# Kernel optimization log

Measured on AMD Instinct MI355X. Metric: run time of the kernel, lower is better.

## Reference

```python
import jax, jax.numpy as jnp
import numpy as np

B, S, D, H = 4, 2048, 1024, 16
HD = D // H

def setup_inputs() -> dict:
    key = jax.random.key(0)
    ks = jax.random.split(key, 5)
    x = jax.random.normal(ks[0], (B, S, D), dtype=jnp.float32)
    # learned params (torch Linear: y = x @ W.T + b)
    s1 = 1.0 / np.sqrt(D)
    Wqkv = jax.random.uniform(ks[1], (3 * D, D), jnp.float32, -s1, s1)
    bqkv = jax.random.uniform(ks[2], (3 * D,), jnp.float32, -s1, s1)
    Wproj = jax.random.uniform(ks[3], (D, D), jnp.float32, -s1, s1)
    bproj = jax.random.uniform(ks[4], (D,), jnp.float32, -s1, s1)
    # causal mask, broadcast over batch and heads; 0 -> masked
    mask = jnp.tril(jnp.ones((S, S), jnp.int32))[None, None]
    return {"x": x, "Wqkv": Wqkv, "bqkv": bqkv, "Wproj": Wproj, "bproj": bproj, "mask": mask}

def reference(x, Wqkv, bqkv, Wproj, bproj, mask):
    b, s, d = x.shape
    qkv = x @ Wqkv.T + bqkv                      # [B,S,3D]
    qkv = qkv.reshape(b, s, 3, H, HD).transpose(2, 0, 3, 1, 4)  # [3,B,H,S,HD]
    q, k, v = qkv[0], qkv[1], qkv[2]
    scores = jnp.einsum('bhqd,bhkd->bhqk', q, k) / np.sqrt(HD).astype(np.float32)
    scores = jnp.where(mask == 0, -jnp.inf, scores)
    attn = jax.nn.softmax(scores, axis=-1)
    ctx = jnp.einsum('bhqk,bhkd->bhqd', attn, v)  # [B,H,S,HD]
    ctx = ctx.transpose(0, 2, 1, 3).reshape(b, s, d)
    return ctx @ Wproj.T + bproj
```

## Files before the change

kernel.cpp:

```cpp
#include <hip/hip_runtime.h>
#include <stdint.h>

typedef __bf16 bf16;
typedef __bf16 bf16x4 __attribute__((ext_vector_type(4)));
typedef __bf16 bf16x8 __attribute__((ext_vector_type(8)));
typedef float f32x4 __attribute__((ext_vector_type(4)));
typedef short short4v __attribute__((ext_vector_type(4)));

#define NB 4
#define NS 2048
#define ND 1024
#define NH 16
#define NHD 64
#define QSCALE 0.1803368801111204f
#define FMAX   8.0f
#define CPITCH 136

typedef const __attribute__((address_space(1))) unsigned GU;
typedef __attribute__((address_space(3))) unsigned LU;

__device__ __forceinline__ bf16x8 load8f(const float* p) {
    float4 a = *(const float4*)p;
    float4 b = *(const float4*)(p + 4);
    bf16x8 r;
    r[0] = (bf16)a.x; r[1] = (bf16)a.y; r[2] = (bf16)a.z; r[3] = (bf16)a.w;
    r[4] = (bf16)b.x; r[5] = (bf16)b.y; r[6] = (bf16)b.z; r[7] = (bf16)b.w;
    return r;
}
__device__ __forceinline__ void store8(bf16* p, bf16x8 v) { *(bf16x8*)p = v; }
__device__ __forceinline__ void store8(float* p, bf16x8 v) {
    float4 a; a.x = (float)v[0]; a.y = (float)v[1]; a.z = (float)v[2]; a.w = (float)v[3];
    float4 b; b.x = (float)v[4]; b.y = (float)v[5]; b.z = (float)v[6]; b.w = (float)v[7];
    *(float4*)p = a; *(float4*)(p + 4) = b;
}

__device__ __forceinline__ f32x4 mfma16(bf16x4 a, bf16x4 b, f32x4 c) {
#ifdef __HIP_DEVICE_COMPILE__
#if __has_builtin(__builtin_amdgcn_mfma_f32_16x16x16bf16_1k)
    return __builtin_amdgcn_mfma_f32_16x16x16bf16_1k(
        __builtin_bit_cast(short4v, a), __builtin_bit_cast(short4v, b), c, 0, 0, 0);
#else
    f32x4 d;
    asm("v_mfma_f32_16x16x16_bf16 %0, %1, %2, %3"
        : "=v"(d) : "v"(a), "v"(b), "v"(c));
    return d;
#endif
#else
    return c;
#endif
}

__device__ __forceinline__ int sw(int row, int col) {
    return row * 72 + (col ^ (((row >> 2) & 3) * 16));
}

__global__ __launch_bounds__(256)
void convert_kernel(const float* __restrict__ s0, bf16* __restrict__ d0, int n0,
                    const float* __restrict__ s1, bf16* __restrict__ d1, int n1,
                    const float* __restrict__ s2, bf16* __restrict__ d2, int n2)
{
    int idx = (blockIdx.x * 256 + threadIdx.x) * 8;
    const float* s; bf16* d;
    if (idx < n0)              { s = s0 + idx;  d = d0 + idx; }
    else if ((idx -= n0) < n1) { s = s1 + idx;  d = d1 + idx; }
    else if ((idx -= n1) < n2) { s = s2 + idx;  d = d2 + idx; }
    else return;
    *(bf16x8*)d = load8f(s);
}

template<typename TO, int MODE>
__device__ __forceinline__ void gemm_epilogue(
    f32x4 (&acc)[4][4], bf16* Ls, const float* __restrict__ bias,
    TO* __restrict__ O0, bf16* __restrict__ O1, bf16* __restrict__ O2,
    int N, int m0, int n0, int tid)
{
    const int lane = tid & 63;
    const int w = tid >> 6, wm = w >> 1, wn = w & 1;
    const int lr = lane & 15, quad = lane >> 4;
    const int cls = (MODE == 0) ? (n0 >> 10) : 1;

    if (MODE == 0 && cls == 2) {
#pragma unroll
        for (int im = 0; im < 4; ++im) {
            int rowb = wm * 64 + im * 16 + quad * 4;
#pragma unroll
            for (int in = 0; in < 4; ++in) {
                int col = wn * 64 + in * 16 + lr;
                float bv = bias[n0 + col];
                bf16x4 pv;
#pragma unroll
                for (int r = 0; r < 4; ++r) pv[r] = (bf16)(acc[im][in][r] + bv);
                *(bf16x4*)&Ls[col * CPITCH + rowb] = pv;
            }
        }
        __syncthreads();
        const int b = m0 >> 11, s0 = m0 & 2047;
#pragma unroll
        for (int p = 0; p < 8; ++p) {
            int idx = tid + 256 * p;
            int col = idx & 127, mg = idx >> 7;
            bf16x8 v8 = *(const bf16x8*)&Ls[col * CPITCH + mg * 8];
            int ncol = n0 + col;
            int h = (ncol >> 6) & 15, hd = ncol & 63;
            *(bf16x8*)&((bf16*)O0)[((size_t)(b * NH + h) * NHD + hd) * NS + s0 + mg * 8] = v8;
        }
    } else {
#pragma unroll
        for (int im = 0; im < 4; ++im) {
            int rowb = wm * 64 + im * 16 + quad * 4;
#pragma unroll
            for (int in = 0; in < 4; ++in) {
                int col = wn * 64 + in * 16 + lr;
                float bv = bias[n0 + col];
#pragma unroll
                for (int r = 0; r < 4; ++r) {
                    float v = acc[im][in][r] + bv;
                    if (MODE == 0 && cls == 0) v *= QSCALE;
                    Ls[(rowb + r) * CPITCH + col] = (bf16)v;
                }
            }
        }
        __syncthreads();
#pragma unroll
        for (int p = 0; p < 8; ++p) {
            int idx = tid + 256 * p;
            int row = idx >> 4, colg = (idx & 15) * 8;
            bf16x8 v8 = *(const bf16x8*)&Ls[row * CPITCH + colg];
            if (MODE == 0) {
                int ncol = n0 + colg;
                int h = (ncol >> 6) & 15, hd = ncol & 63;
                int m = m0 + row, b = m >> 11, s = m & 2047;
                bf16* dst = (cls == 0) ? O1 : O2;
                *(bf16x8*)&dst[((size_t)(b * NH + h) * NS + s) * NHD + hd] = v8;
            } else {
                store8(&O0[(size_t)(m0 + row) * N + n0 + colg], v8);
            }
        }
    }
}

template<typename TO, int MODE>
__global__ __launch_bounds__(256, 3)
void gemm_bt(const bf16* __restrict__ Xp, const bf16* __restrict__ Wp,
             const float* __restrict__ bias, TO* __restrict__ O0,
             bf16* __restrict__ O1, bf16* __restrict__ O2, int N, int K)
{
    __shared__ union {
        struct { bf16 Ah[128 * 32]; bf16 Bh[128 * 32]; } s;
        bf16 C[128 * CPITCH];
    } u;
    const int tid  = threadIdx.x;
    const int lane = tid & 63;
    const int w    = tid >> 6;
    const int wm   = w >> 1, wn = w & 1;
    const int lr   = lane & 15, quad = lane >> 4;
    const int m0   = blockIdx.y * 128;
    const int n0   = blockIdx.x * 128;

    const int srow = w * 32 + (lane >> 2);
    const int scol = (lane & 3) * 8;
    const bf16* gA = Xp + (size_t)(m0 + srow) * K + scol;
    const bf16* gB = Wp + (size_t)(n0 + srow) * K + scol;

    f32x4 acc[4][4] = {};

    for (int k0 = 0; k0 < K; k0 += 32) {
#pragma unroll
        for (int c = 0; c < 2; ++c) {
            __builtin_amdgcn_global_load_lds((GU*)(gA + (size_t)c * 16 * K + k0),
                                             (LU*)&u.s.Ah[(w * 32 + c * 16) * 32], 16, 0, 0);
            __builtin_amdgcn_global_load_lds((GU*)(gB + (size_t)c * 16 * K + k0),
                                             (LU*)&u.s.Bh[(w * 32 + c * 16) * 32], 16, 0, 0);
        }
        __syncthreads();

        bf16x8 af[4], bfr[4];
#pragma unroll
        for (int im = 0; im < 4; ++im)
            af[im] = *(const bf16x8*)(&u.s.Ah[(wm * 64 + im * 16 + lr) * 32 + quad * 8]);
#pragma unroll
        for (int in = 0; in < 4; ++in)
            bfr[in] = *(const bf16x8*)(&u.s.Bh[(wn * 64 + in * 16 + lr) * 32 + quad * 8]);
#pragma unroll
        for (int im = 0; im < 4; ++im)
#pragma unroll
            for (int in = 0; in < 4; ++in)
                acc[im][in] = __builtin_amdgcn_mfma_f32_16x16x32_bf16(
                    af[im], bfr[in], acc[im][in], 0, 0, 0);
        __syncthreads();
    }

    gemm_epilogue<TO, MODE>(acc, u.C, bias, O0, O1, O2, N, m0, n0, tid);
}

__global__ __launch_bounds__(256, 5)
void attn_kernel(const bf16* __restrict__ Q, const bf16* __restrict__ K,
                 const bf16* __restrict__ Vt_g, bf16* __restrict__ ctx)
{
    const int jt = 31 - (blockIdx.x >> 6);
    const int bh = blockIdx.x & 63;
    const int b  = bh >> 4, h = bh & 15;
    const int q0 = jt * 64;
    const bf16* Qp = Q + (size_t)bh * NS * NHD;
    const bf16* Kp = K + (size_t)bh * NS * NHD;
    const bf16* Vp = Vt_g + (size_t)bh * NHD * NS;

    __shared__ bf16 Qh[64 * 72];
    __shared__ bf16 Kh[64 * 72];
    __shared__ bf16 Vh[64 * 72];

    const int tid  = threadIdx.x;
    const int lane = tid & 63;
    const int w    = tid >> 6;
    const int lr   = lane & 15, quad = lane >> 4;

#pragma unroll
    for (int i = 0; i < 2; ++i) {
        int c = tid + 256 * i;
        int row = c >> 3, ch = c & 7;
        *(bf16x8*)(&Qh[sw(row, ch * 8)]) =
            *(const bf16x8*)(Qp + (size_t)(q0 + row) * NHD + ch * 8);
    }

    const int qrow = q0 + w * 16 + lr;
    float l_part = 0.f;
    f32x4 acco[4] = {};

    const int nkt = jt + 1;
    for (int kt = 0; kt < nkt; ++kt) {
        __syncthreads();
#pragma unroll
        for (int i = 0; i < 2; ++i) {
            int c = tid + 256 * i;
            int row = c >> 3, ch = c & 7;
            *(bf16x8*)(&Kh[sw(row, ch * 8)]) =
                *(const bf16x8*)(Kp + (size_t)(kt * 64 + row) * NHD + ch * 8);
            *(bf16x8*)(&Vh[sw(row, ch * 8)]) =
                *(const bf16x8*)(Vp + (size_t)row * NS + kt * 64 + ch * 8);
        }
        __syncthreads();

        f32x4 sacc[4] = {};
#pragma unroll
        for (int ks = 0; ks < 2; ++ks) {
            bf16x8 bq = *(const bf16x8*)(&Qh[sw(w * 16 + lr, ks * 32 + quad * 8)]);
#pragma unroll
            for (int kn = 0; kn < 4; ++kn) {
                bf16x8 ak = *(const bf16x8*)(&Kh[sw(kn * 16 + lr, ks * 32 + quad * 8)]);
                sacc[kn] = __builtin_amdgcn_mfma_f32_16x16x32_bf16(ak, bq, sacc[kn], 0, 0, 0);
            }
        }

        const bool diag = (kt == jt);
        bf16x4 pf[4];
#pragma unroll
        for (int kn = 0; kn < 4; ++kn) {
#pragma unroll
            for (int r = 0; r < 4; ++r) {
                float x = sacc[kn][r];
                if (diag) {
                    int kcol = kt * 64 + kn * 16 + quad * 4 + r;
                    x = (kcol <= qrow) ? x : -INFINITY;
                }
                float p = __builtin_amdgcn_exp2f(x - FMAX);
                l_part += p;
                pf[kn][r] = (bf16)p;
            }
        }

#pragma unroll
        for (int kn = 0; kn < 4; ++kn) {
#pragma unroll
            for (int jn = 0; jn < 4; ++jn) {
                bf16x4 av = *(const bf16x4*)(&Vh[sw(jn * 16 + lr, kn * 16 + quad * 4)]);
                acco[jn] = mfma16(av, pf[kn], acco[jn]);
            }
        }
    }

    float l = l_part;
    l += __shfl_xor(l, 16);
    l += __shfl_xor(l, 32);
    float rinv = 1.0f / l;

    __syncthreads();
#pragma unroll
    for (int jn = 0; jn < 4; ++jn) {
        bf16x4 pv;
#pragma unroll
        for (int r = 0; r < 4; ++r) pv[r] = (bf16)(acco[jn][r] * rinv);
        *(bf16x4*)&Qh[(w * 16 + lr) * 72 + jn * 16 + quad * 4] = pv;
    }
    __syncthreads();
#pragma unroll
    for (int p = 0; p < 2; ++p) {
        int idx = tid + 256 * p;
        int row = idx >> 3, colg = (idx & 7) * 8;
        bf16x8 v8 = *(const bf16x8*)&Qh[row * 72 + colg];
        *(bf16x8*)&ctx[((size_t)(b * NS) + q0 + row) * ND + h * NHD + colg] = v8;
    }
}

extern "C" void kernel_launch(void* const* d_in, const int* in_sizes, int n_in,
                              void* d_out, int out_size, void* d_ws, size_t ws_size,
                              hipStream_t stream) {
    const float* x     = (const float*)d_in[0];
    const float* Wqkv  = (const float*)d_in[1];
    const float* bqkv  = (const float*)d_in[2];
    const float* Wproj = (const float*)d_in[3];
    const float* bproj = (const float*)d_in[4];
    float* out = (float*)d_out;

    const size_t per = (size_t)NB * NH * NS * NHD;
    bf16* q_ws = (bf16*)d_ws;
    bf16* k_ws = q_ws + per;
    bf16* v_ws = k_ws + per;
    bf16* x_bf = v_ws + per;
    bf16* c_ws = x_bf;
    bf16* wq_bf = x_bf + per;
    bf16* wp_bf = wq_bf + (size_t)3 * ND * ND;

    const int n0 = NB * NS * ND;
    const int n1 = 3 * ND * ND;
    const int n2 = ND * ND;
    convert_kernel<<<(n0 + n1 + n2) / (256 * 8), 256, 0, stream>>>(
        x, x_bf, n0, Wqkv, wq_bf, n1, Wproj, wp_bf, n2);

    dim3 gq(3 * ND / 128, NB * NS / 128);
    gemm_bt<bf16, 0><<<gq, 256, 0, stream>>>(
        x_bf, wq_bf, bqkv, v_ws, q_ws, k_ws, 3 * ND, ND);

    attn_kernel<<<dim3(NB * NH * 32), 256, 0, stream>>>(q_ws, k_ws, v_ws, c_ws);

    dim3 gp(ND / 128, NB * NS / 128);
    gemm_bt<float, 1><<<gp, 256, 0, stream>>>(
        c_ws, wp_bf, bproj, out, nullptr, nullptr, ND, ND);
}
```

Baseline: 279.9 us.

## Process 128 query rows per attention block to reuse K/V tiles

Each attention block now handles two 64-row query tiles (128 rows), so each wave keeps two sets of accumulators and shares every loaded K/V tile between both halves. This halves the number of K/V global loads and LDS staging passes per query row and halves the grid size. The cost is more registers per thread (launch bounds lowered from 5 to 4 waves per SIMD), fewer blocks for load balancing across CUs, and a divergence-free but uniform branch for the first half's final step.

```diff
diff --git a/kernel.cpp b/kernel.cpp
--- a/kernel.cpp
+++ b/kernel.cpp
@@ -193,19 +193,19 @@
     gemm_epilogue<TO, MODE>(acc, u.C, bias, O0, O1, O2, N, m0, n0, tid);
 }
 
-__global__ __launch_bounds__(256, 5)
+__global__ __launch_bounds__(256, 4)
 void attn_kernel(const bf16* __restrict__ Q, const bf16* __restrict__ K,
                  const bf16* __restrict__ Vt_g, bf16* __restrict__ ctx)
 {
-    const int jt = 31 - (blockIdx.x >> 6);
+    const int jtp = 15 - (int)(blockIdx.x >> 6);
     const int bh = blockIdx.x & 63;
     const int b  = bh >> 4, h = bh & 15;
-    const int q0 = jt * 64;
+    const int q0 = jtp * 128;
     const bf16* Qp = Q + (size_t)bh * NS * NHD;
     const bf16* Kp = K + (size_t)bh * NS * NHD;
     const bf16* Vp = Vt_g + (size_t)bh * NHD * NS;
 
-    __shared__ bf16 Qh[64 * 72];
+    __shared__ bf16 Qh[128 * 72];
     __shared__ bf16 Kh[64 * 72];
     __shared__ bf16 Vh[64 * 72];
 
@@ -215,18 +215,19 @@
     const int lr   = lane & 15, quad = lane >> 4;
 
 #pragma unroll
-    for (int i = 0; i < 2; ++i) {
+    for (int i = 0; i < 4; ++i) {
         int c = tid + 256 * i;
         int row = c >> 3, ch = c & 7;
         *(bf16x8*)(&Qh[sw(row, ch * 8)]) =
             *(const bf16x8*)(Qp + (size_t)(q0 + row) * NHD + ch * 8);
     }
 
-    const int qrow = q0 + w * 16 + lr;
-    float l_part = 0.f;
-    f32x4 acco[4] = {};
-
-    const int nkt = jt + 1;
+    const int qrow0 = q0 + w * 16 + lr;
+    const int qrow1 = qrow0 + 64;
+    float l0 = 0.f, l1 = 0.f;
+    f32x4 acco0[4] = {}, acco1[4] = {};
+
+    const int nkt = 2 * jtp + 2;
     for (int kt = 0; kt < nkt; ++kt) {
         __syncthreads();
 #pragma unroll
@@ -240,31 +241,42 @@
         }
         __syncthreads();
 
-        f32x4 sacc[4] = {};
+        const bool act0 = (kt <= 2 * jtp);
+
+        f32x4 sacc0[4] = {}, sacc1[4] = {};
 #pragma unroll
         for (int ks = 0; ks < 2; ++ks) {
-            bf16x8 bq = *(const bf16x8*)(&Qh[sw(w * 16 + lr, ks * 32 + quad * 8)]);
+            bf16x8 bq0 = *(const bf16x8*)(&Qh[sw(w * 16 + lr, ks * 32 + quad * 8)]);
+            bf16x8 bq1 = *(const bf16x8*)(&Qh[sw(64 + w * 16 + lr, ks * 32 + quad * 8)]);
 #pragma unroll
             for (int kn = 0; kn < 4; ++kn) {
                 bf16x8 ak = *(const bf16x8*)(&Kh[sw(kn * 16 + lr, ks * 32 + quad * 8)]);
-                sacc[kn] = __builtin_amdgcn_mfma_f32_16x16x32_bf16(ak, bq, sacc[kn], 0, 0, 0);
-            }
-        }
-
-        const bool diag = (kt == jt);
-        bf16x4 pf[4];
+                if (act0)
+                    sacc0[kn] = __builtin_amdgcn_mfma_f32_16x16x32_bf16(ak, bq0, sacc0[kn], 0, 0, 0);
+                sacc1[kn] = __builtin_amdgcn_mfma_f32_16x16x32_bf16(ak, bq1, sacc1[kn], 0, 0, 0);
+            }
+        }
+
+        const bool diag0 = (kt == 2 * jtp);
+        const bool diag1 = (kt == 2 * jtp + 1);
+        bf16x4 pf0[4], pf1[4];
 #pragma unroll
         for (int kn = 0; kn < 4; ++kn) {
 #pragma unroll
             for (int r = 0; r < 4; ++r) {
-                float x = sacc[kn][r];
-                if (diag) {
-                    int kcol = kt * 64 + kn * 16 + quad * 4 + r;
-                    x = (kcol <= qrow) ? x : -INFINITY;
+                int kcol = kt * 64 + kn * 16 + quad * 4 + r;
+                if (act0) {
+                    float x = sacc0[kn][r];
+                    if (diag0) x = (kcol <= qrow0) ? x : -INFINITY;
+                    float p = __builtin_amdgcn_exp2f(x - FMAX);
+                    l0 += p;
+                    pf0[kn][r] = (bf16)p;
                 }
-                float p = __builtin_amdgcn_exp2f(x - FMAX);
-                l_part += p;
-                pf[kn][r] = (bf16)p;
+                float y = sacc1[kn][r];
+                if (diag1) y = (kcol <= qrow1) ? y : -INFINITY;
+                float p1 = __builtin_amdgcn_exp2f(y - FMAX);
+                l1 += p1;
+                pf1[kn][r] = (bf16)p1;
             }
         }
 
@@ -273,27 +285,31 @@
 #pragma unroll
             for (int jn = 0; jn < 4; ++jn) {
                 bf16x4 av = *(const bf16x4*)(&Vh[sw(jn * 16 + lr, kn * 16 + quad * 4)]);
-                acco[jn] = mfma16(av, pf[kn], acco[jn]);
-            }
-        }
-    }
-
-    float l = l_part;
-    l += __shfl_xor(l, 16);
-    l += __shfl_xor(l, 32);
-    float rinv = 1.0f / l;
+                if (act0) acco0[jn] = mfma16(av, pf0[kn], acco0[jn]);
+                acco1[jn] = mfma16(av, pf1[kn], acco1[jn]);
+            }
+        }
+    }
+
+    l0 += __shfl_xor(l0, 16); l0 += __shfl_xor(l0, 32);
+    l1 += __shfl_xor(l1, 16); l1 += __shfl_xor(l1, 32);
+    float rinv0 = 1.0f / l0, rinv1 = 1.0f / l1;
 
     __syncthreads();
 #pragma unroll
     for (int jn = 0; jn < 4; ++jn) {
-        bf16x4 pv;
-#pragma unroll
-        for (int r = 0; r < 4; ++r) pv[r] = (bf16)(acco[jn][r] * rinv);
-        *(bf16x4*)&Qh[(w * 16 + lr) * 72 + jn * 16 + quad * 4] = pv;
+        bf16x4 p0, p1;
+#pragma unroll
+        for (int r = 0; r < 4; ++r) {
+            p0[r] = (bf16)(acco0[jn][r] * rinv0);
+            p1[r] = (bf16)(acco1[jn][r] * rinv1);
+        }
+        *(bf16x4*)&Qh[(w * 16 + lr) * 72 + jn * 16 + quad * 4] = p0;
+        *(bf16x4*)&Qh[(64 + w * 16 + lr) * 72 + jn * 16 + quad * 4] = p1;
     }
     __syncthreads();
 #pragma unroll
-    for (int p = 0; p < 2; ++p) {
+    for (int p = 0; p < 4; ++p) {
         int idx = tid + 256 * p;
         int row = idx >> 3, colg = (idx & 7) * 8;
         bf16x8 v8 = *(const bf16x8*)&Qh[row * 72 + colg];
@@ -330,7 +346,7 @@
     gemm_bt<bf16, 0><<<gq, 256, 0, stream>>>(
         x_bf, wq_bf, bqkv, v_ws, q_ws, k_ws, 3 * ND, ND);
 
-    attn_kernel<<<dim3(NB * NH * 32), 256, 0, stream>>>(q_ws, k_ws, v_ws, c_ws);
+    attn_kernel<<<dim3(NB * NH * 16), 256, 0, stream>>>(q_ws, k_ws, v_ws, c_ws);
 
     dim3 gp(ND / 128, NB * NS / 128);
     gemm_bt<float, 1><<<gp, 256, 0, stream>>>(
```

Result: slower. 306.4 us (+9.5%).
